# Kernel optimization log

Hardware: AMD Instinct MI355X
Metric: run time of the kernel (lower is better)

## Reference

```python
import jax, jax.numpy as jnp
import numpy as np

H = 64  # hidden size hard-coded in the torch module


def _lstm_cell(x, h, c, Wih, Whh, b):
    # PyTorch LSTMCell: gates = x @ Wih.T + h @ Whh.T + bias_ih + bias_hh,
    # gate order (i, f, g, o), each of size H.
    gates = x @ Wih.T + h @ Whh.T + b
    i, f, g, o = jnp.split(gates, 4, axis=-1)
    c_new = jax.nn.sigmoid(f) * c + jax.nn.sigmoid(i) * jnp.tanh(g)
    h_new = jax.nn.sigmoid(o) * jnpp_tanh(c_new) if False else jax.nn.sigmoid(o) * jnp.tanh(c_new)
    return h_new, c_new


def setup_inputs() -> dict:
    key = jax.random.key(0)
    ks = jax.random.split(key, 12)
    B, T, F = 2048, 1024, 1
    s = 1.0 / np.sqrt(H)  # PyTorch LSTMCell/Linear init range

    def u(k, shape):
        return jax.random.uniform(k, shape, jnp.float32, -s, s)

    return {
        "input": jax.random.normal(ks[0], (B, T, F), jnp.float32),
        "Wih1": u(ks[1], (4 * H, F)),
        "Whh1": u(ks[2], (4 * H, H)),
        "bih1": u(ks[3], (4 * H,)),
        "bhh1": u(ks[4], (4 * H,)),
        "Wih2": u(ks[5], (4 * H, H)),
        "Whh2": u(ks[6], (4 * H, H)),
        "bih2": u(ks[7], (4 * H,)),
        "bhh2": u(ks[8], (4 * H,)),
        "Wl": u(ks[9], (1, H)),
        "bl": u(ks[10], (1,)),
        "future": 8,
    }


def reference(input, Wih1, Whh1, bih1, bhh1, Wih2, Whh2, bih2, bhh2, Wl, bl, future):
    B = input.shape[0]
    dtype = input.dtype
    z = jnp.zeros((B, H), dtype)
    b1 = bih1 + bhh1
    b2 = bih2 + bhh2

    def step(carry, x_t):
        h1, c1, h2, c2 = carry
        h1, c1 = _lstm_cell(x_t, h1, c1, Wih1, Whh1, b1)
        h2, c2 = _lstm_cell(h1, h2, c2, Wih2, Whh2, b2)
        return (h1, c1, h2, c2), None

    # scan over time: xs shaped [T, B, F]
    (h1, c1, h2, c2), _ = jax.lax.scan(step, (z, z, z, z), jnp.swapaxes(input, 0, 1))
    out = h2 @ Wl.T + bl  # readout from last input step

    def fstep(carry, _):
        out, h1, c1, h2, c2 = carry
        h1, c1 = _lstm_cell(out, h1, c1, Wih1, Whh1, b1)
        h2, c2 = _lstm_cell(h1, h2, c2, Wih2, Whh2, b2)
        out = h2 @ Wl.T + bl
        return (out, h1, c1, h2, c2), None

    (out, h1, c1, h2, c2), _ = jax.lax.scan(fstep, (out, h1, c1, h2, c2), None, length=future)
    return out[:, None, :]  # [B, 1, out_feature]
```

## Files before the change

kernel.cpp:

```cpp
#include <hip/hip_runtime.h>

#define HID 64
#define TSTEPS 1024
#define BPW 8
#define TW 512

typedef __attribute__((ext_vector_type(8))) short short8v;
typedef __attribute__((ext_vector_type(4))) float f32x4;

__device__ __forceinline__ unsigned short f2bf(float f) {
  unsigned u = __float_as_uint(f);
  u += 0x7FFFu + ((u >> 16) & 1u);
  return (unsigned short)(u >> 16);
}
__device__ __forceinline__ float bf2f(unsigned short h) {
  return __uint_as_float(((unsigned)h) << 16);
}
__device__ __forceinline__ float sigf(float x) {
  return __builtin_amdgcn_rcpf(1.0f + __expf(-x));
}
__device__ __forceinline__ float tanh_(float x) {
  return 1.0f - 2.0f * __builtin_amdgcn_rcpf(1.0f + __expf(2.0f * x));
}
__device__ __forceinline__ float dppror8(float x) {
  int xi = __float_as_int(x);
  int y = __builtin_amdgcn_update_dpp(xi, xi, 0x128, 0xF, 0xF, true);
  return __int_as_float(y);
}
__device__ __forceinline__ f32x4 mf(short8v a, short8v b, f32x4 c) {
  return __builtin_amdgcn_mfma_f32_16x16x32_bf16(a, b, c, 0, 0, 0);
}
__device__ __forceinline__ unsigned cvtpk_bf16(float a) {
  unsigned r;
  asm("v_cvt_pk_bf16_f32 %0, %1, %2" : "=v"(r) : "v"(a), "v"(a));
  return r;
}
__device__ __forceinline__ short8v ld_frag(const short* buf, int ss, int lane) {
  int byte = (ss * 64 + lane) * 16;
  byte ^= ((byte >> 7) & 7) << 4;
  return *(const short8v*)((const char*)buf + byte);
}
__device__ __forceinline__ int frag_addr16(int j, int col) {
  int byte = ((j >> 5) * 64 + ((j & 31) >> 3) * 16 + col) * 16 + (j & 7) * 2;
  byte ^= ((byte >> 7) & 7) << 4;
  return byte;
}
__device__ __forceinline__ void load8split(const float* rp, short8v& hi, short8v& lo) {
  float t[8];
#pragma unroll
  for (int e = 0; e < 8; ++e) t[e] = rp[e];
#pragma unroll
  for (int e = 0; e < 8; ++e) {
    unsigned short h = f2bf(t[e]);
    hi[e] = (short)h;
    lo[e] = (short)f2bf(t[e] - bf2f(h));
  }
}
__device__ __forceinline__ float cellup(float zi, float zf, float zg, float zo,
                                        float& c) {
  c = sigf(zf) * c + sigf(zi) * tanh_(zg);
  return sigf(zo) * tanh_(c);
}
__device__ __forceinline__ void fold2(const f32x4& a0, const f32x4& a1,
                                      bool dsel, float (&z)[4]) {
#pragma unroll
  for (int q = 0; q < 4; ++q) {
    float send = dsel ? a0[q] : a1[q];
    float own = dsel ? a1[q] : a0[q];
    z[q] = own + dppror8(send);
  }
}

struct __align__(128) SMem {
  float xin[TSTEPS][BPW];
  short hf1[2][1024];
  short hf2[2][1024];
  float ro[8][BPW];
};

#define PINV(v) asm volatile("" : "+v"(v))

__global__ __launch_bounds__(TW, 2) void lstm2_kernel(
    const float* __restrict__ input, const float* __restrict__ Wih1,
    const float* __restrict__ Whh1, const float* __restrict__ bih1,
    const float* __restrict__ bhh1, const float* __restrict__ Wih2,
    const float* __restrict__ Whh2, const float* __restrict__ bih2,
    const float* __restrict__ bhh2, const float* __restrict__ Wl,
    const float* __restrict__ bl, const int* __restrict__ future,
    float* __restrict__ out) {
  __shared__ SMem s;
  const int tid = threadIdx.x;
  const int w = tid >> 6;
  const int lane = tid & 63;
  const int c = lane & 15;
  const int b = c & 7;
  const int d = (c >> 3) & 1;
  const int g = lane >> 4;
  const int jl = 4 * (2 * w + d) + g;
  const int b0 = blockIdx.x * BPW;

  short8v W1h[2][2], W1l[2][2];
  short8v W2h[2][2], W2l[2][2];
  short8v W3h[2][2], W3l[2][2];
#pragma unroll
  for (int tt = 0; tt < 2; ++tt) {
    const int T = 2 * w + tt;
    const int r16 = lane & 15;
    const int m = 64 * (r16 & 3) + 4 * T + (r16 >> 2);
    const int koff = (lane >> 4) * 8;
#pragma unroll
    for (int ss = 0; ss < 2; ++ss) {
      load8split(Whh1 + m * HID + ss * 32 + koff, W1h[tt][ss], W1l[tt][ss]);
      load8split(Wih2 + m * HID + ss * 32 + koff, W2h[tt][ss], W2l[tt][ss]);
      load8split(Whh2 + m * HID + ss * 32 + koff, W3h[tt][ss], W3l[tt][ss]);
    }
  }
#pragma unroll
  for (int tt = 0; tt < 2; ++tt)
#pragma unroll
    for (int ss = 0; ss < 2; ++ss) {
      PINV(W1h[tt][ss]); PINV(W1l[tt][ss]);
      PINV(W2h[tt][ss]); PINV(W2l[tt][ss]);
      PINV(W3h[tt][ss]); PINV(W3l[tt][ss]);
    }

  float bb1[4], wi1[4], bb2[4];
#pragma unroll
  for (int q = 0; q < 4; ++q) {
    const int row = 64 * q + jl;
    bb1[q] = bih1[row] + bhh1[row];
    wi1[q] = Wih1[row];
    bb2[q] = bih2[row] + bhh2[row];
  }
  const float wlv = Wl[jl];
  const float blv = bl[0];
  const int nfut = future[0];
  const int adr_hi = frag_addr16(jl, b);
  const int adr_lo = frag_addr16(jl, b + 8);

  {
    const float* src = input + (size_t)b0 * TSTEPS;
    for (int idx = tid; idx < BPW * TSTEPS; idx += TW) {
      int bi = idx >> 10;
      int t = idx & (TSTEPS - 1);
      s.xin[t][bi] = src[idx];
    }
    for (int idx = tid; idx < 2 * 1024; idx += TW) {
      ((short*)s.hf1)[idx] = 0;
      ((short*)s.hf2)[idx] = 0;
    }
  }
  const f32x4 zf = (f32x4){0.f, 0.f, 0.f, 0.f};
  float c1 = 0.f, c2 = 0.f;
  __syncthreads();

  const int total = TSTEPS + nfut;
  for (int i = 0; i <= total; ++i) {
    const int p = i & 1, pn = p ^ 1;
    const bool doL1 = (i < total);
    const bool doL2 = (i >= 1);
    const bool fut = (i >= TSTEPS);

    short8v C0 = ld_frag(s.hf1[p], 0, lane);
    short8v C1 = ld_frag(s.hf1[p], 1, lane);
    short8v B0 = ld_frag(s.hf2[p], 0, lane);
    short8v B1 = ld_frag(s.hf2[p], 1, lane);

    f32x4 a1_0 = mf(W1h[0][1], C1,
                    mf(W1l[0][1], C1, mf(W1h[0][0], C0, mf(W1l[0][0], C0, zf))));
    f32x4 a1_1 = mf(W1h[1][1], C1,
                    mf(W1l[1][1], C1, mf(W1h[1][0], C0, mf(W1l[1][0], C0, zf))));
    f32x4 aA_0 = mf(W3h[0][1], B1,
                    mf(W3l[0][1], B1, mf(W3h[0][0], B0, mf(W3l[0][0], B0, zf))));
    f32x4 aA_1 = mf(W3h[1][1], B1,
                    mf(W3l[1][1], B1, mf(W3h[1][0], B0, mf(W3l[1][0], B0, zf))));
    f32x4 aB_0 = mf(W2h[0][1], C1,
                    mf(W2l[0][1], C1, mf(W2h[0][0], C0, mf(W2l[0][0], C0, zf))));
    f32x4 aB_1 = mf(W2h[1][1], C1,
                    mf(W2l[1][1], C1, mf(W2h[1][0], C0, mf(W2l[1][0], C0, zf))));

    if (doL2) {
      f32x4 s0 = aA_0 + aB_0;
      f32x4 s1 = aA_1 + aB_1;
      float z[4];
      fold2(s0, s1, d, z);
#pragma unroll
      for (int q = 0; q < 4; ++q) z[q] += bb2[q];
      float h2n = cellup(z[0], z[1], z[2], z[3], c2);
      unsigned rh = cvtpk_bf16(h2n);
      float res = h2n - __uint_as_float(rh << 16);
      unsigned rl = cvtpk_bf16(res);
      char* hf2w = (char*)s.hf2[pn];
      *(short*)(hf2w + adr_hi) = (short)rh;
      *(short*)(hf2w + adr_lo) = (short)rl;
      if (fut) {
        float v = wlv * h2n;
        v += __shfl_xor(v, 8, 64);
        v += __shfl_xor(v, 16, 64);
        v += __shfl_xor(v, 32, 64);
        if (lane < 8) s.ro[w][lane] = v;
      }
    }

    float x = 0.0f;
    if (fut) {
      __syncthreads();
      float t = blv;
#pragma unroll
      for (int k = 0; k < 8; ++k) t += s.ro[k][b];
      x = t;
    } else {
      x = s.xin[i][b];
    }

    if (doL1) {
      float z[4];
      fold2(a1_0, a1_1, d, z);
#pragma unroll
      for (int q = 0; q < 4; ++q) z[q] += bb1[q] + x * wi1[q];
      float h1n = cellup(z[0], z[1], z[2], z[3], c1);
      unsigned rh = cvtpk_bf16(h1n);
      float res = h1n - __uint_as_float(rh << 16);
      unsigned rl = cvtpk_bf16(res);
      char* hf1w = (char*)s.hf1[pn];
      *(short*)(hf1w + adr_hi) = (short)rh;
      *(short*)(hf1w + adr_lo) = (short)rl;
    }
    __syncthreads();
  }

  if (tid < 8) {
    float t = blv;
#pragma unroll
    for (int k = 0; k < 8; ++k) t += s.ro[k][tid];
    out[b0 + tid] = t;
  }
}

extern "C" void kernel_launch(void* const* d_in, const int* in_sizes, int n_in,
                              void* d_out, int out_size, void* d_ws,
                              size_t ws_size, hipStream_t stream) {
  const float* input = (const float*)d_in[0];
  const float* Wih1 = (const float*)d_in[1];
  const float* Whh1 = (const float*)d_in[2];
  const float* bih1 = (const float*)d_in[3];
  const float* bhh1 = (const float*)d_in[4];
  const float* Wih2 = (const float*)d_in[5];
  const float* Whh2 = (const float*)d_in[6];
  const float* bih2 = (const float*)d_in[7];
  const float* bhh2 = (const float*)d_in[8];
  const float* Wl = (const float*)d_in[9];
  const float* bl = (const float*)d_in[10];
  const int* fut = (const int*)d_in[11];
  float* out = (float*)d_out;

  const int B = in_sizes[0] / TSTEPS;
  const int blocks = B / BPW;

  hipLaunchKernelGGL(lstm2_kernel, dim3(blocks), dim3(TW), 0, stream, input,
                     Wih1, Whh1, bih1, bhh1, Wih2, Whh2, bih2, bhh2, Wl, bl,
                     fut, out);
}
```

Before: 948.1 us.

## Split LSTM layers into producer/consumer wave groups with LDS flag synchronization

The block grows to 16 waves. Eight waves compute layer 1 and eight compute layer 2, handing data through a 4-deep ring of h1 buffers. Workgroup-scope atomic counters with spin-waits replace the per-step __syncthreads, so layer 1 can run up to three steps ahead of layer 2 and the two recurrences overlap in time. The future-step feedback goes through an xfut buffer and an x_ready flag. In exchange, spin-wait and atomic overhead are added, the block is larger, the launch-bound waves per SIMD change, and register pressure per wave shifts.

```diff
diff --git a/kernel.cpp b/kernel.cpp
--- a/kernel.cpp
+++ b/kernel.cpp
@@ -3,7 +3,7 @@
 #define HID 64
 #define TSTEPS 1024
 #define BPW 8
-#define TW 512
+#define TW 1024
 
 typedef __attribute__((ext_vector_type(8))) short short8v;
 typedef __attribute__((ext_vector_type(4))) float f32x4;
@@ -35,10 +35,10 @@
   asm("v_cvt_pk_bf16_f32 %0, %1, %2" : "=v"(r) : "v"(a), "v"(a));
   return r;
 }
-__device__ __forceinline__ short8v ld_frag(const short* buf, int ss, int lane) {
+__device__ __forceinline__ int frag_ld_off(int ss, int lane) {
   int byte = (ss * 64 + lane) * 16;
   byte ^= ((byte >> 7) & 7) << 4;
-  return *(const short8v*)((const char*)buf + byte);
+  return byte;
 }
 __device__ __forceinline__ int frag_addr16(int j, int col) {
   int byte = ((j >> 5) * 64 + ((j & 31) >> 3) * 16 + col) * 16 + (j & 7) * 2;
@@ -71,16 +71,30 @@
   }
 }
 
+__device__ __forceinline__ void spin_ge(int* p, int tgt) {
+  if (__hip_atomic_load(p, __ATOMIC_ACQUIRE, __HIP_MEMORY_SCOPE_WORKGROUP) < tgt) {
+    while (__hip_atomic_load(p, __ATOMIC_ACQUIRE,
+                             __HIP_MEMORY_SCOPE_WORKGROUP) < tgt)
+      __builtin_amdgcn_s_sleep(1);
+  }
+  __builtin_amdgcn_sched_barrier(0);
+}
+__device__ __forceinline__ void bump(int* p, int lane) {
+  asm volatile("s_waitcnt lgkmcnt(0)" ::: "memory");
+  if (lane == 0)
+    __hip_atomic_fetch_add(p, 1, __ATOMIC_RELEASE, __HIP_MEMORY_SCOPE_WORKGROUP);
+}
+
 struct __align__(128) SMem {
   float xin[TSTEPS][BPW];
-  short hf1[2][1024];
+  short hf1[4][1024];
   short hf2[2][1024];
-  float ro[8][BPW];
+  float xfut[16][BPW];
+  float ro[2][8][BPW];
+  int h1_done, h2_done, x_ready;
 };
 
-#define PINV(v) asm volatile("" : "+v"(v))
-
-__global__ __launch_bounds__(TW, 2) void lstm2_kernel(
+__global__ __launch_bounds__(TW, 4) void lstm2_kernel(
     const float* __restrict__ input, const float* __restrict__ Wih1,
     const float* __restrict__ Whh1, const float* __restrict__ bih1,
     const float* __restrict__ bhh1, const float* __restrict__ Wih2,
@@ -92,51 +106,22 @@
   const int tid = threadIdx.x;
   const int w = tid >> 6;
   const int lane = tid & 63;
+  const int gid = w >> 3;
+  const int v = w & 7;
   const int c = lane & 15;
   const int b = c & 7;
   const int d = (c >> 3) & 1;
   const int g = lane >> 4;
-  const int jl = 4 * (2 * w + d) + g;
+  const int jl = 4 * (2 * v + d) + g;
   const int b0 = blockIdx.x * BPW;
-
-  short8v W1h[2][2], W1l[2][2];
-  short8v W2h[2][2], W2l[2][2];
-  short8v W3h[2][2], W3l[2][2];
-#pragma unroll
-  for (int tt = 0; tt < 2; ++tt) {
-    const int T = 2 * w + tt;
-    const int r16 = lane & 15;
-    const int m = 64 * (r16 & 3) + 4 * T + (r16 >> 2);
-    const int koff = (lane >> 4) * 8;
-#pragma unroll
-    for (int ss = 0; ss < 2; ++ss) {
-      load8split(Whh1 + m * HID + ss * 32 + koff, W1h[tt][ss], W1l[tt][ss]);
-      load8split(Wih2 + m * HID + ss * 32 + koff, W2h[tt][ss], W2l[tt][ss]);
-      load8split(Whh2 + m * HID + ss * 32 + koff, W3h[tt][ss], W3l[tt][ss]);
-    }
-  }
-#pragma unroll
-  for (int tt = 0; tt < 2; ++tt)
-#pragma unroll
-    for (int ss = 0; ss < 2; ++ss) {
-      PINV(W1h[tt][ss]); PINV(W1l[tt][ss]);
-      PINV(W2h[tt][ss]); PINV(W2l[tt][ss]);
-      PINV(W3h[tt][ss]); PINV(W3l[tt][ss]);
-    }
-
-  float bb1[4], wi1[4], bb2[4];
-#pragma unroll
-  for (int q = 0; q < 4; ++q) {
-    const int row = 64 * q + jl;
-    bb1[q] = bih1[row] + bhh1[row];
-    wi1[q] = Wih1[row];
-    bb2[q] = bih2[row] + bhh2[row];
-  }
-  const float wlv = Wl[jl];
+  const int nfut = future[0];
+  const int total = TSTEPS + nfut;
   const float blv = bl[0];
-  const int nfut = future[0];
   const int adr_hi = frag_addr16(jl, b);
   const int adr_lo = frag_addr16(jl, b + 8);
+  const int off0 = frag_ld_off(0, lane);
+  const int off1 = frag_ld_off(1, lane);
+  const f32x4 zf = (f32x4){0.f, 0.f, 0.f, 0.f};
 
   {
     const float* src = input + (size_t)b0 * TSTEPS;
@@ -145,95 +130,148 @@
       int t = idx & (TSTEPS - 1);
       s.xin[t][bi] = src[idx];
     }
-    for (int idx = tid; idx < 2 * 1024; idx += TW) {
-      ((short*)s.hf1)[idx] = 0;
-      ((short*)s.hf2)[idx] = 0;
-    }
-  }
-  const f32x4 zf = (f32x4){0.f, 0.f, 0.f, 0.f};
-  float c1 = 0.f, c2 = 0.f;
+    for (int idx = tid; idx < 4 * 1024; idx += TW) ((short*)s.hf1)[idx] = 0;
+    for (int idx = tid; idx < 2 * 1024; idx += TW) ((short*)s.hf2)[idx] = 0;
+    if (tid == 0) {
+      s.h1_done = 0;
+      s.h2_done = 0;
+      s.x_ready = 0;
+    }
+  }
   __syncthreads();
 
-  const int total = TSTEPS + nfut;
-  for (int i = 0; i <= total; ++i) {
-    const int p = i & 1, pn = p ^ 1;
-    const bool doL1 = (i < total);
-    const bool doL2 = (i >= 1);
-    const bool fut = (i >= TSTEPS);
-
-    short8v C0 = ld_frag(s.hf1[p], 0, lane);
-    short8v C1 = ld_frag(s.hf1[p], 1, lane);
-    short8v B0 = ld_frag(s.hf2[p], 0, lane);
-    short8v B1 = ld_frag(s.hf2[p], 1, lane);
-
-    f32x4 a1_0 = mf(W1h[0][1], C1,
-                    mf(W1l[0][1], C1, mf(W1h[0][0], C0, mf(W1l[0][0], C0, zf))));
-    f32x4 a1_1 = mf(W1h[1][1], C1,
-                    mf(W1l[1][1], C1, mf(W1h[1][0], C0, mf(W1l[1][0], C0, zf))));
-    f32x4 aA_0 = mf(W3h[0][1], B1,
-                    mf(W3l[0][1], B1, mf(W3h[0][0], B0, mf(W3l[0][0], B0, zf))));
-    f32x4 aA_1 = mf(W3h[1][1], B1,
-                    mf(W3l[1][1], B1, mf(W3h[1][0], B0, mf(W3l[1][0], B0, zf))));
-    f32x4 aB_0 = mf(W2h[0][1], C1,
-                    mf(W2l[0][1], C1, mf(W2h[0][0], C0, mf(W2l[0][0], C0, zf))));
-    f32x4 aB_1 = mf(W2h[1][1], C1,
-                    mf(W2l[1][1], C1, mf(W2h[1][0], C0, mf(W2l[1][0], C0, zf))));
-
-    if (doL2) {
-      f32x4 s0 = aA_0 + aB_0;
-      f32x4 s1 = aA_1 + aB_1;
+  if (gid == 0) {
+    short8v Ah[2][2], Al[2][2];
+#pragma unroll
+    for (int tt = 0; tt < 2; ++tt) {
+      const int T = 2 * v + tt;
+      const int r16 = lane & 15;
+      const int m = 64 * (r16 & 3) + 4 * T + (r16 >> 2);
+      const int koff = (lane >> 4) * 8;
+#pragma unroll
+      for (int ss = 0; ss < 2; ++ss)
+        load8split(Whh1 + m * HID + ss * 32 + koff, Ah[tt][ss], Al[tt][ss]);
+    }
+    float bb1[4], wi1[4];
+#pragma unroll
+    for (int q = 0; q < 4; ++q) {
+      const int row = 64 * q + jl;
+      bb1[q] = bih1[row] + bhh1[row];
+      wi1[q] = Wih1[row];
+    }
+    float c1 = 0.f;
+    for (int i = 0; i < total; ++i) {
+      spin_ge(&s.h1_done, 8 * i);
+      if (i >= 4) spin_ge(&s.h2_done, 8 * (i - 3));
+      const char* cb = (const char*)s.hf1[(i - 1) & 3];
+      short8v C0 = *(const short8v*)(cb + off0);
+      short8v C1 = *(const short8v*)(cb + off1);
+      f32x4 a0 = mf(Ah[0][1], C1,
+                    mf(Al[0][1], C1, mf(Ah[0][0], C0, mf(Al[0][0], C0, zf))));
+      f32x4 a1 = mf(Ah[1][1], C1,
+                    mf(Al[1][1], C1, mf(Ah[1][0], C0, mf(Al[1][0], C0, zf))));
+      float x;
+      if (i < TSTEPS) {
+        x = s.xin[i][b];
+      } else {
+        spin_ge(&s.x_ready, i - TSTEPS + 1);
+        x = s.xfut[i - TSTEPS][b];
+      }
       float z[4];
-      fold2(s0, s1, d, z);
+      fold2(a0, a1, d, z);
+#pragma unroll
+      for (int q = 0; q < 4; ++q) z[q] += bb1[q] + x * wi1[q];
+      float h1n = cellup(z[0], z[1], z[2], z[3], c1);
+      unsigned rh = cvtpk_bf16(h1n);
+      float res = h1n - __uint_as_float(rh << 16);
+      unsigned rl = cvtpk_bf16(res);
+      char* hw = (char*)s.hf1[i & 3];
+      *(short*)(hw + adr_hi) = (short)rh;
+      *(short*)(hw + adr_lo) = (short)rl;
+      bump(&s.h1_done, lane);
+    }
+  } else {
+    short8v Ah[2][2], Al[2][2];
+    short8v Bh[2][2], Bl[2][2];
+#pragma unroll
+    for (int tt = 0; tt < 2; ++tt) {
+      const int T = 2 * v + tt;
+      const int r16 = lane & 15;
+      const int m = 64 * (r16 & 3) + 4 * T + (r16 >> 2);
+      const int koff = (lane >> 4) * 8;
+#pragma unroll
+      for (int ss = 0; ss < 2; ++ss) {
+        load8split(Wih2 + m * HID + ss * 32 + koff, Ah[tt][ss], Al[tt][ss]);
+        load8split(Whh2 + m * HID + ss * 32 + koff, Bh[tt][ss], Bl[tt][ss]);
+      }
+    }
+    float bb2[4];
+#pragma unroll
+    for (int q = 0; q < 4; ++q) {
+      const int row = 64 * q + jl;
+      bb2[q] = bih2[row] + bhh2[row];
+    }
+    const float wlv = Wl[jl];
+    float c2 = 0.f;
+    for (int j = 0; j < total; ++j) {
+      spin_ge(&s.h2_done, 8 * j);
+      spin_ge(&s.h1_done, 8 * (j + 1));
+      const char* cb = (const char*)s.hf1[j & 3];
+      short8v C0 = *(const short8v*)(cb + off0);
+      short8v C1 = *(const short8v*)(cb + off1);
+      const char* db = (const char*)s.hf2[(j - 1) & 1];
+      short8v D0 = *(const short8v*)(db + off0);
+      short8v D1 = *(const short8v*)(db + off1);
+      f32x4 a0 = mf(
+          Bh[0][1], D1,
+          mf(Bl[0][1], D1,
+             mf(Bh[0][0], D0,
+                mf(Bl[0][0], D0,
+                   mf(Ah[0][1], C1,
+                      mf(Al[0][1], C1,
+                         mf(Ah[0][0], C0, mf(Al[0][0], C0, zf))))))));
+      f32x4 a1 = mf(
+          Bh[1][1], D1,
+          mf(Bl[1][1], D1,
+             mf(Bh[1][0], D0,
+                mf(Bl[1][0], D0,
+                   mf(Ah[1][1], C1,
+                      mf(Al[1][1], C1,
+                         mf(Ah[1][0], C0, mf(Al[1][0], C0, zf))))))));
+      float z[4];
+      fold2(a0, a1, d, z);
 #pragma unroll
       for (int q = 0; q < 4; ++q) z[q] += bb2[q];
       float h2n = cellup(z[0], z[1], z[2], z[3], c2);
       unsigned rh = cvtpk_bf16(h2n);
       float res = h2n - __uint_as_float(rh << 16);
       unsigned rl = cvtpk_bf16(res);
-      char* hf2w = (char*)s.hf2[pn];
-      *(short*)(hf2w + adr_hi) = (short)rh;
-      *(short*)(hf2w + adr_lo) = (short)rl;
-      if (fut) {
-        float v = wlv * h2n;
-        v += __shfl_xor(v, 8, 64);
-        v += __shfl_xor(v, 16, 64);
-        v += __shfl_xor(v, 32, 64);
-        if (lane < 8) s.ro[w][lane] = v;
+      char* hw = (char*)s.hf2[j & 1];
+      *(short*)(hw + adr_hi) = (short)rh;
+      *(short*)(hw + adr_lo) = (short)rl;
+      if (j >= TSTEPS - 1) {
+        float rv = wlv * h2n;
+        rv += __shfl_xor(rv, 8, 64);
+        rv += __shfl_xor(rv, 16, 64);
+        rv += __shfl_xor(rv, 32, 64);
+        if (lane < 8) s.ro[j & 1][v][lane] = rv;
       }
-    }
-
-    float x = 0.0f;
-    if (fut) {
-      __syncthreads();
-      float t = blv;
-#pragma unroll
-      for (int k = 0; k < 8; ++k) t += s.ro[k][b];
-      x = t;
-    } else {
-      x = s.xin[i][b];
-    }
-
-    if (doL1) {
-      float z[4];
-      fold2(a1_0, a1_1, d, z);
-#pragma unroll
-      for (int q = 0; q < 4; ++q) z[q] += bb1[q] + x * wi1[q];
-      float h1n = cellup(z[0], z[1], z[2], z[3], c1);
-      unsigned rh = cvtpk_bf16(h1n);
-      float res = h1n - __uint_as_float(rh << 16);
-      unsigned rl = cvtpk_bf16(res);
-      char* hf1w = (char*)s.hf1[pn];
-      *(short*)(hf1w + adr_hi) = (short)rh;
-      *(short*)(hf1w + adr_lo) = (short)rl;
-    }
-    __syncthreads();
-  }
-
-  if (tid < 8) {
-    float t = blv;
-#pragma unroll
-    for (int k = 0; k < 8; ++k) t += s.ro[k][tid];
-    out[b0 + tid] = t;
+      bump(&s.h2_done, lane);
+      if (v == 0 && j >= TSTEPS - 1) {
+        spin_ge(&s.h2_done, 8 * (j + 1));
+        float t = blv;
+        if (lane < 8) {
+#pragma unroll
+          for (int k = 0; k < 8; ++k) t += s.ro[j & 1][k][lane];
+        }
+        if (j == total - 1) {
+          if (lane < 8) out[b0 + lane] = t;
+        } else {
+          if (lane < 8) s.xfut[j - (TSTEPS - 1)][lane] = t;
+          bump(&s.x_ready, lane);
+        }
+      }
+    }
   }
 }
 
```

Result: faster. 859.4 us, median of 2 (-9.4%).
